# Performance work log

Hardware: AMD Instinct MI355X
Metric: run time of the kernel (lower is better)

Reference implementation:

```python
import jax, jax.numpy as jnp
import numpy as np

DIM = 256      # dim_hidden * 2
HEADS = 8      # hier_tf_head
C = 256        # out_channels per head (concat=False)
FF = 1024      # dim_hidden * 8
N_HOPS = 4096
HOP_LEN = 12
N_MEM = N_HOPS * HOP_LEN
N = N_HOPS + N_MEM  # 53248 total nodes


def setup_inputs() -> dict:
    key = jax.random.key(0)
    ks = jax.random.split(key, 8)
    x = jax.random.normal(ks[0], (N, DIM), jnp.float32)
    # hop_attn structure built by the python loops: [j,j] self-edges for hop
    # tokens, then one edge (member_node -> hop_token) per member.
    hop_self = np.stack([np.arange(N_HOPS), np.arange(N_HOPS)])
    mem_src = np.arange(N_HOPS, N)
    mem_dst = np.arange(N_MEM) // HOP_LEN
    edge_index = jnp.asarray(
        np.concatenate([hop_self, np.stack([mem_src, mem_dst])], axis=1),
        jnp.int32)  # [2, E]

    def init(k, shp, fan):
        return jax.random.normal(k, shp, jnp.float32) / np.sqrt(fan).astype(np.float32)

    return {
        "x": x,
        "edge_index": edge_index,
        "gat_W": init(ks[1], (DIM, HEADS * C), DIM),
        "gat_att_src": init(ks[2], (HEADS, C), C),
        "gat_att_dst": init(ks[3], (HEADS, C), C),
        "gat_bias": jnp.zeros((C,), jnp.float32),
        "ffn_W1": init(ks[4], (DIM, FF), DIM),
        "ffn_b1": jnp.zeros((FF,), jnp.float32),
        "ffn_W2": init(ks[5], (FF, DIM), FF),
        "ffn_b2": jnp.zeros((DIM,), jnp.float32),
        "ln1_g": jnp.ones((DIM,), jnp.float32),
        "ln1_b": jnp.zeros((DIM,), jnp.float32),
        "ln2_g": jnp.ones((DIM,), jnp.float32),
        "ln2_b": jnp.zeros((DIM,), jnp.float32),
    }


def _layer_norm(x, g, b, eps=1e-5):
    mu = jnp.mean(x, axis=-1, keepdims=True)
    var = jnp.mean(jnp.square(x - mu), axis=-1, keepdims=True)
    return (x - mu) * jax.lax.rsqrt(var + eps) * g + b


def _gat_conv(x, src, dst, W, att_src, att_dst, bias):
    # PyG GATConv, concat=False (mean over heads), negative_slope=0.2
    h = (x @ W).reshape(N, HEADS, C)                       # [N,H,C]
    a_s = jnp.einsum('nhc,hc->nh', h, att_src)             # [N,H]
    a_d = jnp.einsum('nhc,hc->nh', h, att_dst)
    e = jax.nn.leaky_relu(a_s[src] + a_d[dst], 0.2)        # [E,H]
    m = jax.ops.segment_max(e, dst, num_segments=N)        # per-dst softmax
    e = jnp.exp(e - m[dst])
    denom = jax.ops.segment_sum(e, dst, num_segments=N)
    alpha = e / (denom[dst] + 1e-16)                       # [E,H]
    agg = jax.ops.segment_sum(h[src] * alpha[:, :, None], dst, num_segments=N)
    return agg.mean(axis=1) + bias                         # [N,DIM]


def reference(x, edge_index, gat_W, gat_att_src, gat_att_dst, gat_bias,
              ffn_W1, ffn_b1, ffn_W2, ffn_b2, ln1_g, ln1_b, ln2_g, ln2_b):
    # GATConv adds self-loops for every node by default
    loops = jnp.arange(N, dtype=edge_index.dtype)
    src = jnp.concatenate([edge_index[0], loops])
    dst = jnp.concatenate([edge_index[1], loops])
    # GAT + residual + LN (dropout is identity at eval)
    g_out = _gat_conv(x, src, dst, gat_W, gat_att_src, gat_att_dst, gat_bias)
    x1 = _layer_norm(g_out + x, ln1_g, ln1_b)
    # FFN + residual + LN
    ff = jax.nn.relu(x1 @ ffn_W1 + ffn_b1) @ ffn_W2 + ffn_b2
    return _layer_norm(ff + x1, ln2_g, ln2_b)
```

## Files before the change

### kernel.cpp

```cpp
#include <hip/hip_runtime.h>
#include <cstdint>
#include <cstddef>

#define N_TOT   53248
#define N_HOPS  4096
#define HOP_LEN 12
#define NHEAD   8
#define FFD     1024
#define CHUNK   8192
#define GLD     384

typedef __bf16 bf16x8 __attribute__((ext_vector_type(8)));
typedef float f32x4 __attribute__((ext_vector_type(4)));

__device__ __forceinline__ unsigned short f2bf(float f) {
    unsigned int u = __float_as_uint(f);
    u += 0x7FFFu + ((u >> 16) & 1u);
    return (unsigned short)(u >> 16);
}
__device__ __forceinline__ float bf2f(unsigned short b) {
    return __uint_as_float((unsigned int)b << 16);
}
__device__ __forceinline__ void gload16(const void* g, void* l) {
    __builtin_amdgcn_global_load_lds(
        (const __attribute__((address_space(1))) void*)g,
        (__attribute__((address_space(3))) void*)l, 16, 0, 0);
}

__global__ __launch_bounds__(256) void prep_w(
    const float* __restrict__ W, const float* __restrict__ att_s,
    const float* __restrict__ att_d, unsigned short* __restrict__ BcT)
{
    int d = blockIdx.x, c = threadIdx.x;
    int wave = c >> 6;
    __shared__ float ps4[4], pd4[4];
    float wm = 0.f;
    for (int h = 0; h < NHEAD; ++h) {
        float w = W[d * 2048 + h * 256 + c];
        wm += w;
        float ps = w * att_s[h * 256 + c];
        float pd = w * att_d[h * 256 + c];
        for (int o = 32; o > 0; o >>= 1) {
            ps += __shfl_xor(ps, o);
            pd += __shfl_xor(pd, o);
        }
        if ((c & 63) == 0) { ps4[wave] = ps; pd4[wave] = pd; }
        __syncthreads();
        if (c == 0) BcT[(256 + h) * 256 + d] = f2bf(ps4[0] + ps4[1] + ps4[2] + ps4[3]);
        if (c == 1) BcT[(264 + h) * 256 + d] = f2bf(pd4[0] + pd4[1] + pd4[2] + pd4[3]);
        __syncthreads();
    }
    BcT[c * 256 + d] = f2bf(wm * 0.125f);
}

__global__ __launch_bounds__(256) void tconv(
    const float* __restrict__ in, unsigned short* __restrict__ out,
    int IS, int OS, int in_zoff, int out_zoff)
{
    __shared__ float t[32][33];
    in  += (size_t)blockIdx.z * in_zoff;
    out += (size_t)blockIdx.z * out_zoff;
    int tx = threadIdx.x, ty = threadIdx.y;
    int c0 = blockIdx.x * 32, r0 = blockIdx.y * 32;
    #pragma unroll
    for (int k = 0; k < 4; ++k)
        t[ty + 8 * k][tx] = in[(size_t)(r0 + ty + 8 * k) * IS + c0 + tx];
    __syncthreads();
    #pragma unroll
    for (int k = 0; k < 4; ++k)
        out[(size_t)(c0 + ty + 8 * k) * OS + r0 + tx] = f2bf(t[tx][ty + 8 * k]);
}

__global__ __launch_bounds__(256) void cvt_bf16(
    const float* __restrict__ in, unsigned short* __restrict__ out, int n4)
{
    int i = blockIdx.x * 256 + threadIdx.x;
    if (i >= n4) return;
    float4 v = ((const float4*)in)[i];
    ushort4 o;
    o.x = f2bf(v.x); o.y = f2bf(v.y); o.z = f2bf(v.z); o.w = f2bf(v.w);
    ((ushort4*)out)[i] = o;
}

__global__ __launch_bounds__(256) void hop_z(
    const unsigned short* __restrict__ xb, const float* __restrict__ gb,
    unsigned short* __restrict__ z)
{
    int j = blockIdx.x, tid = threadIdx.x;
    __shared__ float xr[13][256];
    __shared__ float sm[NHEAD][13];
    __shared__ float walpha[NHEAD][13];
    __shared__ float mxs[NHEAD], invs[NHEAD];

    for (int i = tid; i < 13 * 32; i += 256) {
        int r = i >> 5, c8 = (i & 31) * 8;
        int src = (r == 0) ? j : (N_HOPS + j * HOP_LEN + r - 1);
        uint4 u = *(const uint4*)&xb[(size_t)src * 256 + c8];
        float4 lo, hi;
        lo.x = bf2f((unsigned short)(u.x & 0xFFFF)); lo.y = bf2f((unsigned short)(u.x >> 16));
        lo.z = bf2f((unsigned short)(u.y & 0xFFFF)); lo.w = bf2f((unsigned short)(u.y >> 16));
        hi.x = bf2f((unsigned short)(u.z & 0xFFFF)); hi.y = bf2f((unsigned short)(u.z >> 16));
        hi.z = bf2f((unsigned short)(u.w & 0xFFFF)); hi.w = bf2f((unsigned short)(u.w >> 16));
        *(float4*)&xr[r][c8] = lo;
        *(float4*)&xr[r][c8 + 4] = hi;
    }
    if (tid < NHEAD * 13) {
        int h = tid / 13, k = tid % 13;
        int src = (k == 0) ? j : (N_HOPS + j * HOP_LEN + k - 1);
        float ad = gb[(size_t)j * GLD + 264 + h];
        float v = gb[(size_t)src * GLD + 256 + h] + ad;
        sm[h][k] = v > 0.f ? v : 0.2f * v;
    }
    __syncthreads();
    if (tid < NHEAD) {
        int h = tid;
        float mx = sm[h][0];
        for (int k = 1; k < 13; ++k) mx = fmaxf(mx, sm[h][k]);
        float sum = 2.f * expf(sm[h][0] - mx);
        for (int k = 1; k < 13; ++k) sum += expf(sm[h][k] - mx);
        mxs[h] = mx;
        invs[h] = 0.125f / (sum + 1e-16f);
    }
    __syncthreads();
    if (tid < NHEAD * 13) {
        int h = tid / 13, k = tid % 13;
        walpha[h][k] = (k == 0 ? 2.f : 1.f) * expf(sm[h][k] - mxs[h]) * invs[h];
    }
    __syncthreads();
    for (int h = 0; h < NHEAD; ++h) {
        float acc = 0.f;
        #pragma unroll
        for (int r = 0; r < 13; ++r) acc += walpha[h][r] * xr[r][tid];
        z[((size_t)j * NHEAD + h) * 256 + tid] = f2bf(acc);
    }
}

template <int RELU, int OUT_BF16>
__global__ __launch_bounds__(256) void gemm_bt(
    const unsigned short* __restrict__ A, const unsigned short* __restrict__ BT,
    const float* __restrict__ bias, void* __restrict__ Cout,
    int M, int Nc, int K, int ldc)
{
    __shared__ __align__(16) unsigned short As[128 * 32];
    __shared__ __align__(16) unsigned short Bs[128 * 32];
    const int tid = threadIdx.x;
    const int l = tid & 63;
    const int bm = blockIdx.y * 128, bn = blockIdx.x * 128;
    const int wm = ((tid >> 6) >> 1) * 64, wn = ((tid >> 6) & 1) * 64;

    const int r0 = tid >> 2, ke0 = (tid & 3) * 8;
    const int r1 = (256 + tid) >> 2, ke1 = ((256 + tid) & 3) * 8;
    const unsigned short* ga0 = A + (size_t)(bm + r0) * K + ke0;
    const unsigned short* ga1 = A + (size_t)(bm + r1) * K + ke1;
    const unsigned short* gb0 = BT + (size_t)(bn + r0) * K + ke0;
    const unsigned short* gb1 = BT + (size_t)(bn + r1) * K + ke1;

    f32x4 acc[4][4];
    #pragma unroll
    for (int m = 0; m < 4; ++m)
        #pragma unroll
        for (int n = 0; n < 4; ++n)
            acc[m][n] = (f32x4){0.f, 0.f, 0.f, 0.f};

    const int lrow = l & 15, lk8 = (l >> 4) * 8;

    for (int k0 = 0; k0 < K; k0 += 32) {
        gload16(ga0 + k0, &As[(size_t)tid * 8]);
        gload16(ga1 + k0, &As[(size_t)(256 + tid) * 8]);
        gload16(gb0 + k0, &Bs[(size_t)tid * 8]);
        gload16(gb1 + k0, &Bs[(size_t)(256 + tid) * 8]);
        __syncthreads();
        bf16x8 af[4], bfr[4];
        #pragma unroll
        for (int m = 0; m < 4; ++m)
            af[m] = *(const bf16x8*)&As[(wm + m * 16 + lrow) * 32 + lk8];
        #pragma unroll
        for (int n = 0; n < 4; ++n)
            bfr[n] = *(const bf16x8*)&Bs[(wn + n * 16 + lrow) * 32 + lk8];
        #pragma unroll
        for (int m = 0; m < 4; ++m)
            #pragma unroll
            for (int n = 0; n < 4; ++n)
                acc[m][n] = __builtin_amdgcn_mfma_f32_16x16x32_bf16(
                    af[m], bfr[n], acc[m][n], 0, 0, 0);
        __syncthreads();
    }

    const int orow = (l >> 4) * 4, ocol = l & 15;
    #pragma unroll
    for (int m = 0; m < 4; ++m) {
        int gr = bm + wm + m * 16 + orow;
        #pragma unroll
        for (int n = 0; n < 4; ++n) {
            int gc = bn + wn + n * 16 + ocol;
            float bv = bias[gc];
            #pragma unroll
            for (int r = 0; r < 4; ++r) {
                float v = acc[m][n][r] + bv;
                if (RELU) v = fmaxf(v, 0.f);
                if (OUT_BF16)
                    ((unsigned short*)Cout)[(size_t)(gr + r) * ldc + gc] = f2bf(v);
                else
                    ((float*)Cout)[(size_t)(gr + r) * ldc + gc] = v;
            }
        }
    }
}

__global__ __launch_bounds__(256) void gemm_bt_sk(
    const unsigned short* __restrict__ A, const unsigned short* __restrict__ BT,
    unsigned short* __restrict__ Cpart, int M, int Nc, int Ksl, int ldA)
{
    __shared__ __align__(16) unsigned short As[128 * 32];
    __shared__ __align__(16) unsigned short Bs[128 * 32];
    const int tid = threadIdx.x;
    const int l = tid & 63;
    const int bm = blockIdx.y * 128, bn = blockIdx.x * 128;
    const int koff = blockIdx.z * Ksl;
    const int wm = ((tid >> 6) >> 1) * 64, wn = ((tid >> 6) & 1) * 64;

    const int r0 = tid >> 2, ke0 = (tid & 3) * 8;
    const int r1 = (256 + tid) >> 2, ke1 = ((256 + tid) & 3) * 8;
    const unsigned short* ga0 = A + (size_t)(bm + r0) * ldA + koff + ke0;
    const unsigned short* ga1 = A + (size_t)(bm + r1) * ldA + koff + ke1;
    const unsigned short* gb0 = BT + (size_t)(bn + r0) * ldA + koff + ke0;
    const unsigned short* gb1 = BT + (size_t)(bn + r1) * ldA + koff + ke1;

    f32x4 acc[4][4];
    #pragma unroll
    for (int m = 0; m < 4; ++m)
        #pragma unroll
        for (int n = 0; n < 4; ++n)
            acc[m][n] = (f32x4){0.f, 0.f, 0.f, 0.f};

    const int lrow = l & 15, lk8 = (l >> 4) * 8;

    for (int k0 = 0; k0 < Ksl; k0 += 32) {
        gload16(ga0 + k0, &As[(size_t)tid * 8]);
        gload16(ga1 + k0, &As[(size_t)(256 + tid) * 8]);
        gload16(gb0 + k0, &Bs[(size_t)tid * 8]);
        gload16(gb1 + k0, &Bs[(size_t)(256 + tid) * 8]);
        __syncthreads();
        bf16x8 af[4], bfr[4];
        #pragma unroll
        for (int m = 0; m < 4; ++m)
            af[m] = *(const bf16x8*)&As[(wm + m * 16 + lrow) * 32 + lk8];
        #pragma unroll
        for (int n = 0; n < 4; ++n)
            bfr[n] = *(const bf16x8*)&Bs[(wn + n * 16 + lrow) * 32 + lk8];
        #pragma unroll
        for (int m = 0; m < 4; ++m)
            #pragma unroll
            for (int n = 0; n < 4; ++n)
                acc[m][n] = __builtin_amdgcn_mfma_f32_16x16x32_bf16(
                    af[m], bfr[n], acc[m][n], 0, 0, 0);
        __syncthreads();
    }

    unsigned short* Cp = Cpart + (size_t)blockIdx.z * M * Nc;
    const int orow = (l >> 4) * 4, ocol = l & 15;
    #pragma unroll
    for (int m = 0; m < 4; ++m) {
        int gr = bm + wm + m * 16 + orow;
        #pragma unroll
        for (int n = 0; n < 4; ++n) {
            int gc = bn + wn + n * 16 + ocol;
            #pragma unroll
            for (int r = 0; r < 4; ++r)
                Cp[(size_t)(gr + r) * Nc + gc] = f2bf(acc[m][n][r]);
        }
    }
}

__global__ __launch_bounds__(256) void red_hop(
    const unsigned short* __restrict__ P, const float* __restrict__ bias,
    float* __restrict__ gbuf)
{
    int i = blockIdx.x * 256 + threadIdx.x;
    int row = i >> 6, c4 = (i & 63) * 4;
    float4 s = { 0.f, 0.f, 0.f, 0.f };
    #pragma unroll
    for (int zz = 0; zz < 8; ++zz) {
        ushort4 u = *(const ushort4*)&P[(size_t)zz * N_HOPS * 256 + (size_t)row * 256 + c4];
        s.x += bf2f(u.x); s.y += bf2f(u.y); s.z += bf2f(u.z); s.w += bf2f(u.w);
    }
    float4 bv = *(const float4*)&bias[c4];
    s.x += bv.x; s.y += bv.y; s.z += bv.z; s.w += bv.w;
    *(float4*)&gbuf[(size_t)row * GLD + c4] = s;
}

template <int OUT_BF16>
__global__ __launch_bounds__(256) void ln_add(
    const float* __restrict__ a, int lda4,
    const unsigned short* __restrict__ b,
    const float* __restrict__ g, const float* __restrict__ be,
    void* __restrict__ outv)
{
    int wave = threadIdx.x >> 6, lane = threadIdx.x & 63;
    int n = blockIdx.x * 4 + wave;
    float4 av = ((const float4*)a)[(size_t)n * lda4 + lane];
    ushort4 bv = ((const ushort4*)b)[(size_t)n * 64 + lane];
    float v[4];
    v[0] = av.x + bf2f(bv.x); v[1] = av.y + bf2f(bv.y);
    v[2] = av.z + bf2f(bv.z); v[3] = av.w + bf2f(bv.w);
    float s = v[0] + v[1] + v[2] + v[3];
    for (int o = 32; o > 0; o >>= 1) s += __shfl_xor(s, o);
    float mu = s * (1.f / 256.f);
    float q = 0.f;
    #pragma unroll
    for (int i = 0; i < 4; ++i) { float d = v[i] - mu; q += d * d; }
    for (int o = 32; o > 0; o >>= 1) q += __shfl_xor(q, o);
    float rstd = rsqrtf(q * (1.f / 256.f) + 1e-5f);
    int c = lane * 4;
    float4 gv = *(const float4*)&g[c];
    float4 bev = *(const float4*)&be[c];
    float r0 = (v[0] - mu) * rstd * gv.x + bev.x;
    float r1 = (v[1] - mu) * rstd * gv.y + bev.y;
    float r2 = (v[2] - mu) * rstd * gv.z + bev.z;
    float r3 = (v[3] - mu) * rstd * gv.w + bev.w;
    if (OUT_BF16) {
        ushort4 o4 = { f2bf(r0), f2bf(r1), f2bf(r2), f2bf(r3) };
        ((ushort4*)outv)[(size_t)n * 64 + lane] = o4;
    } else {
        float4 o4 = { r0, r1, r2, r3 };
        ((float4*)outv)[(size_t)n * 64 + lane] = o4;
    }
}

__global__ __launch_bounds__(256) void ln_add_p(
    const unsigned short* __restrict__ P0, const unsigned short* __restrict__ P1,
    const float* __restrict__ b2, const unsigned short* __restrict__ res,
    const float* __restrict__ g, const float* __restrict__ be,
    float* __restrict__ out)
{
    int wave = threadIdx.x >> 6, lane = threadIdx.x & 63;
    int n = blockIdx.x * 4 + wave;
    size_t vidx = (size_t)n * 64 + lane;
    ushort4 p0 = ((const ushort4*)P0)[vidx];
    ushort4 p1 = ((const ushort4*)P1)[vidx];
    ushort4 rv = ((const ushort4*)res)[vidx];
    int c = lane * 4;
    float4 b2v = *(const float4*)&b2[c];
    float v[4];
    v[0] = bf2f(p0.x) + bf2f(p1.x) + b2v.x + bf2f(rv.x);
    v[1] = bf2f(p0.y) + bf2f(p1.y) + b2v.y + bf2f(rv.y);
    v[2] = bf2f(p0.z) + bf2f(p1.z) + b2v.z + bf2f(rv.z);
    v[3] = bf2f(p0.w) + bf2f(p1.w) + b2v.w + bf2f(rv.w);
    float s = v[0] + v[1] + v[2] + v[3];
    for (int o = 32; o > 0; o >>= 1) s += __shfl_xor(s, o);
    float mu = s * (1.f / 256.f);
    float q = 0.f;
    #pragma unroll
    for (int i = 0; i < 4; ++i) { float d = v[i] - mu; q += d * d; }
    for (int o = 32; o > 0; o >>= 1) q += __shfl_xor(q, o);
    float rstd = rsqrtf(q * (1.f / 256.f) + 1e-5f);
    float4 gv = *(const float4*)&g[c];
    float4 bev = *(const float4*)&be[c];
    float4 o4;
    o4.x = (v[0] - mu) * rstd * gv.x + bev.x;
    o4.y = (v[1] - mu) * rstd * gv.y + bev.y;
    o4.z = (v[2] - mu) * rstd * gv.z + bev.z;
    o4.w = (v[3] - mu) * rstd * gv.w + bev.w;
    ((float4*)out)[vidx] = o4;
}

extern "C" void kernel_launch(void* const* d_in, const int* in_sizes, int n_in,
                              void* d_out, int out_size, void* d_ws, size_t ws_size,
                              hipStream_t stream)
{
    const float* x       = (const float*)d_in[0];
    const float* gat_W   = (const float*)d_in[2];
    const float* att_src = (const float*)d_in[3];
    const float* att_dst = (const float*)d_in[4];
    const float* gat_b   = (const float*)d_in[5];
    const float* W1      = (const float*)d_in[6];
    const float* b1      = (const float*)d_in[7];
    const float* W2      = (const float*)d_in[8];
    const float* b2      = (const float*)d_in[9];
    const float* ln1_g   = (const float*)d_in[10];
    const float* ln1_b   = (const float*)d_in[11];
    const float* ln2_g   = (const float*)d_in[12];
    const float* ln2_b   = (const float*)d_in[13];
    float* out = (float*)d_out;

    char* p = (char*)d_ws;
    auto carve = [&p](size_t bytes) { char* r = p; p += (bytes + 255) & ~(size_t)255; return r; };
    float*          gbuf = (float*)carve((size_t)N_TOT * GLD * 4);
    unsigned short* x1b  = (unsigned short*)carve((size_t)N_TOT * 256 * 2);

    size_t fixed_tail = (size_t)GLD * 256 * 2 + (size_t)2048 * 256 * 2 +
                        (size_t)FFD * 256 * 2 + (size_t)256 * FFD * 2 + GLD * 4 + 8 * 256;
    size_t need_full = (size_t)(p - (char*)d_ws) + (size_t)N_TOT * FFD * 2 + fixed_tail;
    bool full = ws_size >= need_full;

    unsigned short* hid  = nullptr;
    unsigned short* z;
    unsigned short* hopP;
    if (full) {
        hid  = (unsigned short*)carve((size_t)N_TOT * FFD * 2);
        z    = hid;
        hopP = hid + (size_t)N_HOPS * 2048;
    } else {
        z    = (unsigned short*)carve((size_t)N_HOPS * 2048 * 2);
        hopP = nullptr;
    }
    unsigned short* BcT  = (unsigned short*)carve((size_t)GLD * 256 * 2);
    unsigned short* B2T  = (unsigned short*)carve((size_t)2048 * 256 * 2);
    unsigned short* W1T  = (unsigned short*)carve((size_t)FFD * 256 * 2);
    unsigned short* W2T  = (unsigned short*)carve((size_t)256 * FFD * 2);
    float*          bias384 = (float*)carve(GLD * 4);
    unsigned short* ffP0 = (unsigned short*)gbuf;
    unsigned short* ffP1 = ffP0 + (size_t)N_TOT * 256;

    hipMemsetAsync(BcT + 272 * 256, 0, (size_t)(GLD - 272) * 256 * 2, stream);
    hipMemcpyAsync(bias384, gat_b, 256 * 4, hipMemcpyDeviceToDevice, stream);
    hipMemsetAsync(bias384 + 256, 0, (GLD - 256) * 4, stream);
    hipLaunchKernelGGL(prep_w, dim3(256), dim3(256), 0, stream,
                       gat_W, att_src, att_dst, BcT);
    hipLaunchKernelGGL(tconv, dim3(8, 8, 8), dim3(32, 8), 0, stream,
                       gat_W, B2T, 2048, 2048, 256, 256);
    hipLaunchKernelGGL(tconv, dim3(32, 8, 1), dim3(32, 8), 0, stream,
                       W1, W1T, 1024, 256, 0, 0);
    hipLaunchKernelGGL(tconv, dim3(8, 32, 1), dim3(32, 8), 0, stream,
                       W2, W2T, 256, 1024, 0, 0);
    hipLaunchKernelGGL(cvt_bf16, dim3(N_TOT * 256 / 4 / 256), dim3(256), 0, stream,
                       x, x1b, N_TOT * 256 / 4);
    hipLaunchKernelGGL((gemm_bt<0, 0>), dim3(GLD / 128, N_TOT / 128), dim3(256), 0, stream,
                       x1b, BcT, bias384, gbuf, N_TOT, GLD, 256, GLD);
    hipLaunchKernelGGL(hop_z, dim3(N_HOPS), dim3(256), 0, stream,
                       x1b, gbuf, z);
    if (full) {
        hipLaunchKernelGGL(gemm_bt_sk, dim3(2, N_HOPS / 128, 8), dim3(256), 0, stream,
                           z, B2T, hopP, N_HOPS, 256, 256, 2048);
        hipLaunchKernelGGL(red_hop, dim3(N_HOPS * 64 / 256), dim3(256), 0, stream,
                           hopP, gat_b, gbuf);
    } else {
        hipLaunchKernelGGL((gemm_bt<0, 0>), dim3(2, N_HOPS / 128), dim3(256), 0, stream,
                           z, B2T, gat_b, gbuf, N_HOPS, 256, 2048, GLD);
    }
    hipLaunchKernelGGL((ln_add<1>), dim3(N_TOT / 4), dim3(256), 0, stream,
                       gbuf, GLD / 4, x1b, ln1_g, ln1_b, x1b);
    if (full) {
        hipLaunchKernelGGL((gemm_bt<1, 1>), dim3(FFD / 128, N_TOT / 128), dim3(256), 0, stream,
                           x1b, W1T, b1, hid, N_TOT, FFD, 256, FFD);
        hipLaunchKernelGGL(gemm_bt_sk, dim3(2, N_TOT / 128, 2), dim3(256), 0, stream,
                           hid, W2T, ffP0, N_TOT, 256, 512, FFD);
        hipLaunchKernelGGL(ln_add_p, dim3(N_TOT / 4), dim3(256), 0, stream,
                           ffP0, ffP1, b2, x1b, ln2_g, ln2_b, out);
    } else {
        unsigned short* hidc = z;
        for (int c0 = 0; c0 < N_TOT; c0 += CHUNK) {
            int Mc = (N_TOT - c0) < CHUNK ? (N_TOT - c0) : CHUNK;
            hipLaunchKernelGGL((gemm_bt<1, 1>), dim3(FFD / 128, Mc / 128), dim3(256), 0, stream,
                               x1b + (size_t)c0 * 256, W1T, b1, hidc, Mc, FFD, 256, FFD);
            hipLaunchKernelGGL((gemm_bt<0, 0>), dim3(2, Mc / 128), dim3(256), 0, stream,
                               hidc, W2T, b2, gbuf + (size_t)c0 * GLD, Mc, 256, FFD, GLD);
        }
        hipLaunchKernelGGL((ln_add<0>), dim3(N_TOT / 4), dim3(256), 0, stream,
                           gbuf, GLD / 4, x1b, ln2_g, ln2_b, out);
    }
    (void)in_sizes; (void)n_in; (void)out_size;
}
```

Before: 259.2 us.

## Fuse FFN GEMMs with bias, ReLU, residual and LayerNorm; store GAT buffer in bf16

Replaces the two FFN GEMM launches plus the split-K partial LayerNorm kernel with a single fused kernel. Each 128-row block computes hidden chunks of 64 columns in LDS, applies bias and ReLU, and accumulates the second GEMM in registers before doing residual add and LayerNorm in the epilogue. This avoids writing and re-reading the large hidden activation tensor through global memory. It also stores the GAT projection/attention buffer as bf16 rather than fp32, cutting its traffic at some cost in precision. The fused kernel re-streams the weight chunks for every row block, its load/compute loop has no double buffering, and the one-pass variance formula is less numerically robust.

```diff
diff --git a/kernel.cpp b/kernel.cpp
--- a/kernel.cpp
+++ b/kernel.cpp
@@ -7,7 +7,6 @@
 #define HOP_LEN 12
 #define NHEAD   8
 #define FFD     1024
-#define CHUNK   8192
 #define GLD     384
 
 typedef __bf16 bf16x8 __attribute__((ext_vector_type(8)));
@@ -83,7 +82,7 @@
 }
 
 __global__ __launch_bounds__(256) void hop_z(
-    const unsigned short* __restrict__ xb, const float* __restrict__ gb,
+    const unsigned short* __restrict__ xb, const unsigned short* __restrict__ gb,
     unsigned short* __restrict__ z)
 {
     int j = blockIdx.x, tid = threadIdx.x;
@@ -107,8 +106,8 @@
     if (tid < NHEAD * 13) {
         int h = tid / 13, k = tid % 13;
         int src = (k == 0) ? j : (N_HOPS + j * HOP_LEN + k - 1);
-        float ad = gb[(size_t)j * GLD + 264 + h];
-        float v = gb[(size_t)src * GLD + 256 + h] + ad;
+        float ad = bf2f(gb[(size_t)j * GLD + 264 + h]);
+        float v = bf2f(gb[(size_t)src * GLD + 256 + h]) + ad;
         sm[h][k] = v > 0.f ? v : 0.2f * v;
     }
     __syncthreads();
@@ -274,7 +273,7 @@
 
 __global__ __launch_bounds__(256) void red_hop(
     const unsigned short* __restrict__ P, const float* __restrict__ bias,
-    float* __restrict__ gbuf)
+    unsigned short* __restrict__ gbuf)
 {
     int i = blockIdx.x * 256 + threadIdx.x;
     int row = i >> 6, c4 = (i & 63) * 4;
@@ -285,24 +284,24 @@
         s.x += bf2f(u.x); s.y += bf2f(u.y); s.z += bf2f(u.z); s.w += bf2f(u.w);
     }
     float4 bv = *(const float4*)&bias[c4];
-    s.x += bv.x; s.y += bv.y; s.z += bv.z; s.w += bv.w;
-    *(float4*)&gbuf[(size_t)row * GLD + c4] = s;
-}
-
-template <int OUT_BF16>
-__global__ __launch_bounds__(256) void ln_add(
-    const float* __restrict__ a, int lda4,
-    const unsigned short* __restrict__ b,
+    ushort4 o;
+    o.x = f2bf(s.x + bv.x); o.y = f2bf(s.y + bv.y);
+    o.z = f2bf(s.z + bv.z); o.w = f2bf(s.w + bv.w);
+    *(ushort4*)&gbuf[(size_t)row * GLD + c4] = o;
+}
+
+__global__ __launch_bounds__(256) void ln_add_bb(
+    const unsigned short* __restrict__ a, const unsigned short* __restrict__ b,
     const float* __restrict__ g, const float* __restrict__ be,
-    void* __restrict__ outv)
+    unsigned short* __restrict__ outp)
 {
     int wave = threadIdx.x >> 6, lane = threadIdx.x & 63;
     int n = blockIdx.x * 4 + wave;
-    float4 av = ((const float4*)a)[(size_t)n * lda4 + lane];
+    ushort4 av = *(const ushort4*)&a[(size_t)n * GLD + lane * 4];
     ushort4 bv = ((const ushort4*)b)[(size_t)n * 64 + lane];
     float v[4];
-    v[0] = av.x + bf2f(bv.x); v[1] = av.y + bf2f(bv.y);
-    v[2] = av.z + bf2f(bv.z); v[3] = av.w + bf2f(bv.w);
+    v[0] = bf2f(av.x) + bf2f(bv.x); v[1] = bf2f(av.y) + bf2f(bv.y);
+    v[2] = bf2f(av.z) + bf2f(bv.z); v[3] = bf2f(av.w) + bf2f(bv.w);
     float s = v[0] + v[1] + v[2] + v[3];
     for (int o = 32; o > 0; o >>= 1) s += __shfl_xor(s, o);
     float mu = s * (1.f / 256.f);
@@ -314,54 +313,195 @@
     int c = lane * 4;
     float4 gv = *(const float4*)&g[c];
     float4 bev = *(const float4*)&be[c];
-    float r0 = (v[0] - mu) * rstd * gv.x + bev.x;
-    float r1 = (v[1] - mu) * rstd * gv.y + bev.y;
-    float r2 = (v[2] - mu) * rstd * gv.z + bev.z;
-    float r3 = (v[3] - mu) * rstd * gv.w + bev.w;
-    if (OUT_BF16) {
-        ushort4 o4 = { f2bf(r0), f2bf(r1), f2bf(r2), f2bf(r3) };
-        ((ushort4*)outv)[(size_t)n * 64 + lane] = o4;
-    } else {
-        float4 o4 = { r0, r1, r2, r3 };
-        ((float4*)outv)[(size_t)n * 64 + lane] = o4;
-    }
-}
-
-__global__ __launch_bounds__(256) void ln_add_p(
-    const unsigned short* __restrict__ P0, const unsigned short* __restrict__ P1,
-    const float* __restrict__ b2, const unsigned short* __restrict__ res,
-    const float* __restrict__ g, const float* __restrict__ be,
-    float* __restrict__ out)
-{
-    int wave = threadIdx.x >> 6, lane = threadIdx.x & 63;
-    int n = blockIdx.x * 4 + wave;
-    size_t vidx = (size_t)n * 64 + lane;
-    ushort4 p0 = ((const ushort4*)P0)[vidx];
-    ushort4 p1 = ((const ushort4*)P1)[vidx];
-    ushort4 rv = ((const ushort4*)res)[vidx];
-    int c = lane * 4;
-    float4 b2v = *(const float4*)&b2[c];
-    float v[4];
-    v[0] = bf2f(p0.x) + bf2f(p1.x) + b2v.x + bf2f(rv.x);
-    v[1] = bf2f(p0.y) + bf2f(p1.y) + b2v.y + bf2f(rv.y);
-    v[2] = bf2f(p0.z) + bf2f(p1.z) + b2v.z + bf2f(rv.z);
-    v[3] = bf2f(p0.w) + bf2f(p1.w) + b2v.w + bf2f(rv.w);
-    float s = v[0] + v[1] + v[2] + v[3];
-    for (int o = 32; o > 0; o >>= 1) s += __shfl_xor(s, o);
-    float mu = s * (1.f / 256.f);
-    float q = 0.f;
-    #pragma unroll
-    for (int i = 0; i < 4; ++i) { float d = v[i] - mu; q += d * d; }
-    for (int o = 32; o > 0; o >>= 1) q += __shfl_xor(q, o);
-    float rstd = rsqrtf(q * (1.f / 256.f) + 1e-5f);
-    float4 gv = *(const float4*)&g[c];
-    float4 bev = *(const float4*)&be[c];
-    float4 o4;
-    o4.x = (v[0] - mu) * rstd * gv.x + bev.x;
-    o4.y = (v[1] - mu) * rstd * gv.y + bev.y;
-    o4.z = (v[2] - mu) * rstd * gv.z + bev.z;
-    o4.w = (v[3] - mu) * rstd * gv.w + bev.w;
-    ((float4*)out)[vidx] = o4;
+    ushort4 o4;
+    o4.x = f2bf((v[0] - mu) * rstd * gv.x + bev.x);
+    o4.y = f2bf((v[1] - mu) * rstd * gv.y + bev.y);
+    o4.z = f2bf((v[2] - mu) * rstd * gv.z + bev.z);
+    o4.w = f2bf((v[3] - mu) * rstd * gv.w + bev.w);
+    ((ushort4*)outp)[(size_t)n * 64 + lane] = o4;
+}
+
+__global__ __launch_bounds__(512, 2) void fused_ffn(
+    const unsigned short* __restrict__ x1b, const unsigned short* __restrict__ W1T,
+    const float* __restrict__ b1, const unsigned short* __restrict__ W2T,
+    const float* __restrict__ b2, const float* __restrict__ g2,
+    const float* __restrict__ be2, float* __restrict__ out)
+{
+    __shared__ __align__(16) unsigned short sX1[8 * 128 * 32];
+    __shared__ __align__(16) unsigned short sW1[8 * 64 * 32];
+    __shared__ __align__(16) unsigned short sW2[2 * 256 * 32];
+    __shared__ __align__(16) unsigned short sH[2 * 128 * 32];
+    __shared__ float lnS[128][4], lnQ[128][4], lnMu[128], lnRs[128];
+
+    const int tid = threadIdx.x, l = tid & 63, wid = tid >> 6;
+    const int lrow = l & 15, hi16 = l >> 4;
+    const int row0 = blockIdx.x * 128;
+    const int wm1 = (wid >> 1) * 32, wn1 = (wid & 1) * 32;
+    const int wm2 = (wid >> 2) * 64, wn2 = (wid & 3) * 64;
+
+    float b2c[4], gc[4], bc[4];
+    #pragma unroll
+    for (int n = 0; n < 4; ++n) {
+        int col = wn2 + n * 16 + lrow;
+        b2c[n] = b2[col]; gc[n] = g2[col]; bc[n] = be2[col];
+    }
+
+    #pragma unroll
+    for (int i = 0; i < 8; ++i) {
+        int c = i * 512 + tid;
+        int s = c >> 9, r = (c >> 2) & 127, q = c & 3;
+        int gq = q ^ (r & 3);
+        gload16(x1b + (size_t)(row0 + r) * 256 + s * 32 + gq * 8, &sX1[c * 8]);
+    }
+    #pragma unroll
+    for (int i = 0; i < 4; ++i) {
+        int c = i * 512 + tid;
+        int s = c >> 8, hc = (c >> 2) & 63, q = c & 3;
+        gload16(W1T + (size_t)hc * 256 + s * 32 + (q ^ (hc & 3)) * 8, &sW1[c * 8]);
+    }
+    #pragma unroll
+    for (int i = 0; i < 4; ++i) {
+        int c = i * 512 + tid;
+        int k2 = c >> 10, fc = (c >> 2) & 255, q = c & 3;
+        gload16(W2T + (size_t)fc * 1024 + k2 * 32 + (q ^ (fc & 3)) * 8, &sW2[c * 8]);
+    }
+    __syncthreads();
+
+    f32x4 facc[4][4];
+    #pragma unroll
+    for (int m = 0; m < 4; ++m)
+        #pragma unroll
+        for (int n = 0; n < 4; ++n)
+            facc[m][n] = (f32x4){0.f, 0.f, 0.f, 0.f};
+
+    const int ra = wm1 + lrow, rb = wm1 + 16 + lrow;
+    const int rc = wn1 + lrow, rd = wn1 + 16 + lrow;
+    const int oa = ((hi16 ^ (ra & 3)) << 3), ob = ((hi16 ^ (rb & 3)) << 3);
+    const int oc = ((hi16 ^ (rc & 3)) << 3), od = ((hi16 ^ (rd & 3)) << 3);
+
+    for (int ch = 0; ch < 16; ++ch) {
+        f32x4 hacc[2][2];
+        #pragma unroll
+        for (int m = 0; m < 2; ++m)
+            #pragma unroll
+            for (int n = 0; n < 2; ++n)
+                hacc[m][n] = (f32x4){0.f, 0.f, 0.f, 0.f};
+        #pragma unroll
+        for (int ks = 0; ks < 8; ++ks) {
+            bf16x8 a0 = *(const bf16x8*)&sX1[ks * 4096 + ra * 32 + oa];
+            bf16x8 a1 = *(const bf16x8*)&sX1[ks * 4096 + rb * 32 + ob];
+            bf16x8 w0 = *(const bf16x8*)&sW1[ks * 2048 + rc * 32 + oc];
+            bf16x8 w1 = *(const bf16x8*)&sW1[ks * 2048 + rd * 32 + od];
+            hacc[0][0] = __builtin_amdgcn_mfma_f32_16x16x32_bf16(a0, w0, hacc[0][0], 0, 0, 0);
+            hacc[0][1] = __builtin_amdgcn_mfma_f32_16x16x32_bf16(a0, w1, hacc[0][1], 0, 0, 0);
+            hacc[1][0] = __builtin_amdgcn_mfma_f32_16x16x32_bf16(a1, w0, hacc[1][0], 0, 0, 0);
+            hacc[1][1] = __builtin_amdgcn_mfma_f32_16x16x32_bf16(a1, w1, hacc[1][1], 0, 0, 0);
+        }
+        #pragma unroll
+        for (int n = 0; n < 2; ++n) {
+            int hcol = wn1 + n * 16 + lrow;
+            float bb = b1[ch * 64 + hcol];
+            int k2 = hcol >> 5, kk = hcol & 31;
+            #pragma unroll
+            for (int m = 0; m < 2; ++m) {
+                #pragma unroll
+                for (int r = 0; r < 4; ++r) {
+                    int row = wm1 + m * 16 + hi16 * 4 + r;
+                    float v = fmaxf(hacc[m][n][r] + bb, 0.f);
+                    sH[k2 * 4096 + row * 32 + ((((kk >> 3) ^ (row & 3)) << 3) | (kk & 7))] = f2bf(v);
+                }
+            }
+        }
+        __syncthreads();
+        #pragma unroll
+        for (int k2 = 0; k2 < 2; ++k2) {
+            bf16x8 a[4];
+            #pragma unroll
+            for (int m = 0; m < 4; ++m) {
+                int r = wm2 + m * 16 + lrow;
+                a[m] = *(const bf16x8*)&sH[k2 * 4096 + r * 32 + ((hi16 ^ (r & 3)) << 3)];
+            }
+            #pragma unroll
+            for (int n = 0; n < 4; ++n) {
+                int r = wn2 + n * 16 + lrow;
+                bf16x8 w = *(const bf16x8*)&sW2[k2 * 8192 + r * 32 + ((hi16 ^ (r & 3)) << 3)];
+                #pragma unroll
+                for (int m = 0; m < 4; ++m)
+                    facc[m][n] = __builtin_amdgcn_mfma_f32_16x16x32_bf16(a[m], w, facc[m][n], 0, 0, 0);
+            }
+        }
+        __syncthreads();
+        if (ch < 15) {
+            int c2 = ch + 1;
+            #pragma unroll
+            for (int i = 0; i < 4; ++i) {
+                int c = i * 512 + tid;
+                int s = c >> 8, hc = (c >> 2) & 63, q = c & 3;
+                gload16(W1T + (size_t)(c2 * 64 + hc) * 256 + s * 32 + (q ^ (hc & 3)) * 8, &sW1[c * 8]);
+            }
+            #pragma unroll
+            for (int i = 0; i < 4; ++i) {
+                int c = i * 512 + tid;
+                int k2 = c >> 10, fc = (c >> 2) & 255, q = c & 3;
+                gload16(W2T + (size_t)fc * 1024 + c2 * 64 + k2 * 32 + (q ^ (fc & 3)) * 8, &sW2[c * 8]);
+            }
+            __syncthreads();
+        }
+    }
+
+    #pragma unroll
+    for (int m = 0; m < 4; ++m) {
+        #pragma unroll
+        for (int n = 0; n < 4; ++n) {
+            int col = wn2 + n * 16 + lrow;
+            int s = col >> 5, kk = col & 31;
+            #pragma unroll
+            for (int r = 0; r < 4; ++r) {
+                int row = wm2 + m * 16 + hi16 * 4 + r;
+                float res = bf2f(sX1[s * 4096 + row * 32 +
+                                     ((((kk >> 3) ^ (row & 3)) << 3) | (kk & 7))]);
+                facc[m][n][r] += b2c[n] + res;
+            }
+        }
+    }
+    #pragma unroll
+    for (int m = 0; m < 4; ++m) {
+        #pragma unroll
+        for (int r = 0; r < 4; ++r) {
+            float s = 0.f, q = 0.f;
+            #pragma unroll
+            for (int n = 0; n < 4; ++n) { float v = facc[m][n][r]; s += v; q += v * v; }
+            #pragma unroll
+            for (int o = 8; o >= 1; o >>= 1) { s += __shfl_xor(s, o); q += __shfl_xor(q, o); }
+            if (lrow == 0) {
+                int row = wm2 + m * 16 + hi16 * 4 + r;
+                lnS[row][wid & 3] = s; lnQ[row][wid & 3] = q;
+            }
+        }
+    }
+    __syncthreads();
+    if (tid < 128) {
+        float s = lnS[tid][0] + lnS[tid][1] + lnS[tid][2] + lnS[tid][3];
+        float q = lnQ[tid][0] + lnQ[tid][1] + lnQ[tid][2] + lnQ[tid][3];
+        float mu = s * (1.f / 256.f);
+        lnMu[tid] = mu;
+        lnRs[tid] = rsqrtf(q * (1.f / 256.f) - mu * mu + 1e-5f);
+    }
+    __syncthreads();
+    #pragma unroll
+    for (int m = 0; m < 4; ++m) {
+        #pragma unroll
+        for (int r = 0; r < 4; ++r) {
+            int row = wm2 + m * 16 + hi16 * 4 + r;
+            float mu = lnMu[row], rs = lnRs[row];
+            #pragma unroll
+            for (int n = 0; n < 4; ++n) {
+                int col = wn2 + n * 16 + lrow;
+                out[(size_t)(row0 + row) * 256 + col] =
+                    (facc[m][n][r] - mu) * rs * gc[n] + bc[n];
+            }
+        }
+    }
 }
 
 extern "C" void kernel_launch(void* const* d_in, const int* in_sizes, int n_in,
@@ -385,32 +525,15 @@
 
     char* p = (char*)d_ws;
     auto carve = [&p](size_t bytes) { char* r = p; p += (bytes + 255) & ~(size_t)255; return r; };
-    float*          gbuf = (float*)carve((size_t)N_TOT * GLD * 4);
+    unsigned short* gbuf = (unsigned short*)carve((size_t)N_TOT * GLD * 2);
     unsigned short* x1b  = (unsigned short*)carve((size_t)N_TOT * 256 * 2);
-
-    size_t fixed_tail = (size_t)GLD * 256 * 2 + (size_t)2048 * 256 * 2 +
-                        (size_t)FFD * 256 * 2 + (size_t)256 * FFD * 2 + GLD * 4 + 8 * 256;
-    size_t need_full = (size_t)(p - (char*)d_ws) + (size_t)N_TOT * FFD * 2 + fixed_tail;
-    bool full = ws_size >= need_full;
-
-    unsigned short* hid  = nullptr;
-    unsigned short* z;
-    unsigned short* hopP;
-    if (full) {
-        hid  = (unsigned short*)carve((size_t)N_TOT * FFD * 2);
-        z    = hid;
-        hopP = hid + (size_t)N_HOPS * 2048;
-    } else {
-        z    = (unsigned short*)carve((size_t)N_HOPS * 2048 * 2);
-        hopP = nullptr;
-    }
+    unsigned short* z    = (unsigned short*)carve((size_t)N_HOPS * 2048 * 2);
+    unsigned short* hopP = (unsigned short*)carve((size_t)8 * N_HOPS * 256 * 2);
     unsigned short* BcT  = (unsigned short*)carve((size_t)GLD * 256 * 2);
     unsigned short* B2T  = (unsigned short*)carve((size_t)2048 * 256 * 2);
     unsigned short* W1T  = (unsigned short*)carve((size_t)FFD * 256 * 2);
     unsigned short* W2T  = (unsigned short*)carve((size_t)256 * FFD * 2);
     float*          bias384 = (float*)carve(GLD * 4);
-    unsigned short* ffP0 = (unsigned short*)gbuf;
-    unsigned short* ffP1 = ffP0 + (size_t)N_TOT * 256;
 
     hipMemsetAsync(BcT + 272 * 256, 0, (size_t)(GLD - 272) * 256 * 2, stream);
     hipMemcpyAsync(bias384, gat_b, 256 * 4, hipMemcpyDeviceToDevice, stream);
@@ -425,39 +548,17 @@
                        W2, W2T, 256, 1024, 0, 0);
     hipLaunchKernelGGL(cvt_bf16, dim3(N_TOT * 256 / 4 / 256), dim3(256), 0, stream,
                        x, x1b, N_TOT * 256 / 4);
-    hipLaunchKernelGGL((gemm_bt<0, 0>), dim3(GLD / 128, N_TOT / 128), dim3(256), 0, stream,
+    hipLaunchKernelGGL((gemm_bt<0, 1>), dim3(GLD / 128, N_TOT / 128), dim3(256), 0, stream,
                        x1b, BcT, bias384, gbuf, N_TOT, GLD, 256, GLD);
     hipLaunchKernelGGL(hop_z, dim3(N_HOPS), dim3(256), 0, stream,
                        x1b, gbuf, z);
-    if (full) {
-        hipLaunchKernelGGL(gemm_bt_sk, dim3(2, N_HOPS / 128, 8), dim3(256), 0, stream,
-                           z, B2T, hopP, N_HOPS, 256, 256, 2048);
-        hipLaunchKernelGGL(red_hop, dim3(N_HOPS * 64 / 256), dim3(256), 0, stream,
-                           hopP, gat_b, gbuf);
-    } else {
-        hipLaunchKernelGGL((gemm_bt<0, 0>), dim3(2, N_HOPS / 128), dim3(256), 0, stream,
-                           z, B2T, gat_b, gbuf, N_HOPS, 256, 2048, GLD);
-    }
-    hipLaunchKernelGGL((ln_add<1>), dim3(N_TOT / 4), dim3(256), 0, stream,
-                       gbuf, GLD / 4, x1b, ln1_g, ln1_b, x1b);
-    if (full) {
-        hipLaunchKernelGGL((gemm_bt<1, 1>), dim3(FFD / 128, N_TOT / 128), dim3(256), 0, stream,
-                           x1b, W1T, b1, hid, N_TOT, FFD, 256, FFD);
-        hipLaunchKernelGGL(gemm_bt_sk, dim3(2, N_TOT / 128, 2), dim3(256), 0, stream,
-                           hid, W2T, ffP0, N_TOT, 256, 512, FFD);
-        hipLaunchKernelGGL(ln_add_p, dim3(N_TOT / 4), dim3(256), 0, stream,
-                           ffP0, ffP1, b2, x1b, ln2_g, ln2_b, out);
-    } else {
-        unsigned short* hidc = z;
-        for (int c0 = 0; c0 < N_TOT; c0 += CHUNK) {
-            int Mc = (N_TOT - c0) < CHUNK ? (N_TOT - c0) : CHUNK;
-            hipLaunchKernelGGL((gemm_bt<1, 1>), dim3(FFD / 128, Mc / 128), dim3(256), 0, stream,
-                               x1b + (size_t)c0 * 256, W1T, b1, hidc, Mc, FFD, 256, FFD);
-            hipLaunchKernelGGL((gemm_bt<0, 0>), dim3(2, Mc / 128), dim3(256), 0, stream,
-                               hidc, W2T, b2, gbuf + (size_t)c0 * GLD, Mc, 256, FFD, GLD);
-        }
-        hipLaunchKernelGGL((ln_add<0>), dim3(N_TOT / 4), dim3(256), 0, stream,
-                           gbuf, GLD / 4, x1b, ln2_g, ln2_b, out);
-    }
-    (void)in_sizes; (void)n_in; (void)out_size;
-}
+    hipLaunchKernelGGL(gemm_bt_sk, dim3(2, N_HOPS / 128, 8), dim3(256), 0, stream,
+                       z, B2T, hopP, N_HOPS, 256, 256, 2048);
+    hipLaunchKernelGGL(red_hop, dim3(N_HOPS * 64 / 256), dim3(256), 0, stream,
+                       hopP, gat_b, gbuf);
+    hipLaunchKernelGGL(ln_add_bb, dim3(N_TOT / 4), dim3(256), 0, stream,
+                       gbuf, x1b, ln1_g, ln1_b, x1b);
+    hipLaunchKernelGGL(fused_ffn, dim3(N_TOT / 128), dim3(512), 0, stream,
+                       x1b, W1T, b1, W2T, b2, ln2_g, ln2_b, out);
+    (void)in_sizes; (void)n_in; (void)out_size; (void)ws_size;
+}
```

Result: faster. 232.9 us (-10.1%).
